# Performance work log

Hardware: AMD Instinct MI355X
Metric: run time of the kernel (lower is better)

Reference implementation:

```python
import jax, jax.numpy as jnp
import numpy as np

N, E = 50000, 800000
MUL, NATTR, NEMB, HID, NPATH = 32, 8, 8, 8, 5
AVG_NEIGH = 16.0
INV3 = 1.0 / np.sqrt(3.0)  # CG norm for 1o x 1o -> 0e (dot)
INV2 = 1.0 / np.sqrt(2.0)  # CG norm for 1o x 1o -> 1o (cross)


def setup_inputs() -> dict:
    key = jax.random.key(0)
    ks = jax.random.split(key, 16)
    f = lambda k, s: jax.random.normal(k, s, jnp.float32)
    return {
        "node_s": f(ks[0], (N, MUL)),
        "node_v": f(ks[1], (N, MUL, 3)),
        "node_attrs": f(ks[2], (N, NATTR)),
        "edge_emb": f(ks[3], (E, NEMB)),
        "edge_sh0": f(ks[4], (E, 1)),
        "edge_sh1": f(ks[5], (E, 3)),
        "W1_s": f(ks[6], (MUL, MUL)),
        "W1_v": f(ks[7], (MUL, MUL)),
        "Wm1": f(ks[8], (NEMB, HID)),
        "Wm2": f(ks[9], (HID, NPATH * MUL)),
        "W2_s": f(ks[10], (2 * MUL, MUL)),
        "W2_v": f(ks[11], (3 * MUL, MUL)),
        "Wsc_s": f(ks[12], (MUL, NATTR, MUL)),
        "Wsc_v": f(ks[13], (MUL, NATTR, MUL)),
        "edge_src": jax.random.randint(ks[14], (E,), 0, N),
        "edge_dst": jax.random.randint(ks[15], (E,), 0, N),
    }


def reference(node_s, node_v, node_attrs, edge_emb, edge_sh0, edge_sh1,
              W1_s, W1_v, Wm1, Wm2, W2_s, W2_v, Wsc_s, Wsc_v,
              edge_src, edge_dst):
    # linear_1: per-l equivariant channel mixing
    x_s = node_s @ W1_s / np.sqrt(MUL)                          # [N, MUL]
    x_v = jnp.einsum('nuc,uv->nvc', node_v, W1_v) / np.sqrt(MUL)  # [N, MUL, 3]
    # gather source node features per edge
    s = x_s[edge_src]   # [E, MUL]
    v = x_v[edge_src]   # [E, MUL, 3]
    # radial MLP on edge embedding -> per-edge UVU tensor-product weights
    h = jax.nn.silu(edge_emb @ Wm1 / np.sqrt(NEMB))
    w = (h @ Wm2 / np.sqrt(HID)).reshape(E, NPATH, MUL)
    w1, w2, w3, w4, w5 = (w[:, i] for i in range(NPATH))
    # UVU Clebsch-Gordan paths (lmax = 1)
    p1 = w1 * s * edge_sh0                                              # 0e x 0e -> 0e
    p2 = w2 * jnp.einsum('euc,ec->eu', v, edge_sh1) * INV3              # 1o x 1o -> 0e
    p3 = w3[:, :, None] * s[:, :, None] * edge_sh1[:, None, :]          # 0e x 1o -> 1o
    p4 = w4[:, :, None] * v * edge_sh0[:, :, None]                      # 1o x 0e -> 1o
    p5 = w5[:, :, None] * jnp.cross(v, edge_sh1[:, None, :]) * INV2     # 1o x 1o -> 1o
    msg_s = jnp.concatenate([p1, p2], axis=1)       # [E, 2*MUL]
    msg_v = jnp.concatenate([p3, p4, p5], axis=1)   # [E, 3*MUL, 3]
    # scatter-add messages to destination nodes
    agg_s = jax.ops.segment_sum(msg_s, edge_dst, num_segments=N)
    agg_v = jax.ops.segment_sum(msg_v, edge_dst, num_segments=N)
    inv = 1.0 / np.sqrt(AVG_NEIGH)
    agg_s = agg_s * inv
    agg_v = agg_v * inv
    # linear_2
    m_s = agg_s @ W2_s / np.sqrt(2 * MUL)
    m_v = jnp.einsum('nuc,uv->nvc', agg_v, W2_v) / np.sqrt(3 * MUL)
    # self connection: fully connected TP with scalar node attrs
    nsc = 1.0 / np.sqrt(MUL * NATTR)
    sc_s = jnp.einsum('nu,na,uav->nv', node_s, node_attrs, Wsc_s) * nsc
    sc_v = jnp.einsum('nuc,na,uav->nvc', node_v, node_attrs, Wsc_v) * nsc
    out_s = m_s + sc_s                  # [N, MUL]
    out_v = m_v + sc_v                  # [N, MUL, 3]
    return jnp.concatenate([out_s, out_v.reshape(N, MUL * 3)], axis=1)  # [N, 128]
```

## Files before the change

### kernel.cpp

```cpp
#include <hip/hip_runtime.h>
#include <math.h>

#define NN 50000
#define NE 800000
#define MUL 32
#define NPB 4
#define SCANB 49

static __device__ __forceinline__ float sigmoidf_(float v) {
    return 1.0f / (1.0f + __expf(-v));
}

#define INV_SQRT_MUL   0.17677669529663687f
#define INV_SQRT_NEMB  0.35355339059327373f
#define INV_SQRT_HID   0.35355339059327373f
#define INV3C          0.5773502691896258f
#define INV2C          0.7071067811865476f
#define INV_NEIGH      0.25f
#define INV_SQRT_2MUL  0.125f
#define INV_SQRT_3MUL  0.10206207261596575f
#define NSC            0.0625f

__global__ __launch_bounds__(256) void k_node(
    const float* __restrict__ node_s, const float* __restrict__ node_v,
    const float* __restrict__ attrs,
    const float* __restrict__ W1_s, const float* __restrict__ W1_v,
    const float* __restrict__ Wsc_s, const float* __restrict__ Wsc_v,
    const int* __restrict__ edge_dst, int* __restrict__ counts,
    float* __restrict__ x, float* __restrict__ out)
{
    __shared__ float nd[NPB][136];
    __shared__ float gs[NPB][1024];
    __shared__ float gv[NPB][1024];
    const int t  = threadIdx.x;
    const int nb = blockIdx.x * NPB;

    {
        int g = blockIdx.x * 256 + t;
        if (g < NE) atomicAdd(&counts[edge_dst[g]], 1);
    }

#pragma unroll
    for (int i = t; i < NPB * 128; i += 256) {
        int nn = i >> 7, j = i & 127;
        nd[nn][j] = (j < 32) ? node_s[(nb + nn) * 32 + j]
                             : node_v[(nb + nn) * 96 + (j - 32)];
    }
    if (t < NPB * 8) nd[t >> 3][128 + (t & 7)] = attrs[(nb + (t >> 3)) * 8 + (t & 7)];
    __syncthreads();

    float at[NPB][8];
#pragma unroll
    for (int nn = 0; nn < NPB; ++nn)
#pragma unroll
        for (int a = 0; a < 8; ++a) at[nn][a] = nd[nn][128 + a];

#pragma unroll
    for (int r = 0; r < 4; ++r) {
        const int idx = t + 256 * r;
        const int u = idx >> 5, vch = idx & 31;
        float as[NPB] = {0.f, 0.f, 0.f, 0.f};
        float av[NPB] = {0.f, 0.f, 0.f, 0.f};
#pragma unroll
        for (int a = 0; a < 8; ++a) {
            const float ws = Wsc_s[(u * 8 + a) * 32 + vch];
            const float wvw = Wsc_v[(u * 8 + a) * 32 + vch];
#pragma unroll
            for (int nn = 0; nn < NPB; ++nn) {
                as[nn] += at[nn][a] * ws;
                av[nn] += at[nn][a] * wvw;
            }
        }
#pragma unroll
        for (int nn = 0; nn < NPB; ++nn) {
            gs[nn][idx] = as[nn];
            gv[nn][idx] = av[nn];
        }
    }
    __syncthreads();

    const int o  = t & 127;
    const int nh = t >> 7;
    if (o < 32) {
        float ax[2] = {0.f, 0.f}, asc[2] = {0.f, 0.f};
#pragma unroll
        for (int uu = 0; uu < 32; ++uu) {
            const float w1 = W1_s[uu * 32 + o];
#pragma unroll
            for (int r2 = 0; r2 < 2; ++r2) {
                const int nn = nh + 2 * r2;
                const float s = nd[nn][uu];
                ax[r2]  += s * w1;
                asc[r2] += s * gs[nn][(uu << 5) + o];
            }
        }
#pragma unroll
        for (int r2 = 0; r2 < 2; ++r2) {
            const int nidx = nb + nh + 2 * r2;
            x[(size_t)nidx * 128 + 4 * o] = ax[r2] * INV_SQRT_MUL;
            out[(size_t)nidx * 128 + o]   = asc[r2] * NSC;
        }
    } else {
        const int q = o - 32;
        const int vch = q / 3, c = q - 3 * vch;
        float ax[2] = {0.f, 0.f}, asc[2] = {0.f, 0.f};
#pragma unroll
        for (int uu = 0; uu < 32; ++uu) {
            const float w1 = W1_v[uu * 32 + vch];
#pragma unroll
            for (int r2 = 0; r2 < 2; ++r2) {
                const int nn = nh + 2 * r2;
                const float vv = nd[nn][32 + 3 * uu + c];
                ax[r2]  += vv * w1;
                asc[r2] += vv * gv[nn][(uu << 5) + vch];
            }
        }
#pragma unroll
        for (int r2 = 0; r2 < 2; ++r2) {
            const int nidx = nb + nh + 2 * r2;
            x[(size_t)nidx * 128 + 4 * vch + 1 + c] = ax[r2] * INV_SQRT_MUL;
            out[(size_t)nidx * 128 + o]             = asc[r2] * NSC;
        }
    }
}

__global__ __launch_bounds__(1024) void k_scan_a(
    const int* __restrict__ counts, int* __restrict__ escan,
    int* __restrict__ bsum)
{
    __shared__ int sh[1024];
    const int t = threadIdx.x;
    const int i = blockIdx.x * 1024 + t;
    int v = (i < NN) ? counts[i] : 0;
    sh[t] = v;
    __syncthreads();
    for (int off = 1; off < 1024; off <<= 1) {
        int u = (t >= off) ? sh[t - off] : 0;
        __syncthreads();
        sh[t] += u;
        __syncthreads();
    }
    if (i < NN) escan[i] = sh[t] - v;
    if (t == 1023) bsum[blockIdx.x] = sh[1023];
}

__global__ __launch_bounds__(1024) void k_scan_c(
    const int* __restrict__ escan, const int* __restrict__ bsum,
    int* __restrict__ offsets, int* __restrict__ cursor)
{
    __shared__ int sbase;
    const int t = threadIdx.x;
    if (t < 64) {
        int v = (t < blockIdx.x) ? bsum[t] : 0;
        for (int off = 32; off > 0; off >>= 1) v += __shfl_xor(v, off, 64);
        if (t == 0) sbase = v;
    }
    __syncthreads();
    const int i = blockIdx.x * 1024 + t;
    if (i == 0) offsets[NN] = NE;
    if (i < NN) {
        int o = sbase + escan[i];
        offsets[i] = o;
        cursor[i] = o;
    }
}

__global__ __launch_bounds__(256) void k_pack(
    const float* __restrict__ edge_emb, const float* __restrict__ edge_sh0,
    const float* __restrict__ edge_sh1,
    const int* __restrict__ edge_src, const int* __restrict__ edge_dst,
    const float* __restrict__ Wm1,
    int* __restrict__ cursor, float* __restrict__ epack)
{
    int e = blockIdx.x * 256 + threadIdx.x;
    if (e >= NE) return;
    const float4* p = (const float4*)(edge_emb + e * 8);
    float4 a = p[0], b = p[1];
    float emb[8] = {a.x, a.y, a.z, a.w, b.x, b.y, b.z, b.w};
    float h[8];
#pragma unroll
    for (int j = 0; j < 8; ++j) {
        float s = 0.f;
#pragma unroll
        for (int k = 0; k < 8; ++k) s += emb[k] * Wm1[k * 8 + j];
        s *= INV_SQRT_NEMB;
        h[j] = s * sigmoidf_(s);
    }
    float sh0 = edge_sh0[e];
    float sx = edge_sh1[3 * e], sy = edge_sh1[3 * e + 1], sz = edge_sh1[3 * e + 2];
    int src = edge_src[e];
    int pos = atomicAdd(&cursor[edge_dst[e]], 1);
    float4* op = (float4*)(epack + (size_t)pos * 16);
    op[0] = make_float4(__int_as_float(src), sh0, sx, sy);
    op[1] = make_float4(sz, h[0], h[1], h[2]);
    op[2] = make_float4(h[3], h[4], h[5], h[6]);
    op[3] = make_float4(h[7], 0.f, 0.f, 0.f);
}

__global__ __launch_bounds__(256) void k_gather(
    const float* __restrict__ x, const float* __restrict__ epack,
    const float* __restrict__ Wm2, const float* __restrict__ W2_s,
    const float* __restrict__ W2_v,
    const int* __restrict__ offsets, float* __restrict__ out)
{
    __shared__ __align__(16) float wsh[2048];
    __shared__ __align__(16) float wvh[3072];
    __shared__ float msg[4][360];

    for (int i = threadIdx.x; i < 512; i += 256)
        ((float4*)wsh)[i] = ((const float4*)W2_s)[i];
    for (int i = threadIdx.x; i < 768; i += 256)
        ((float4*)wvh)[i] = ((const float4*)W2_v)[i];

    const int w    = threadIdx.x >> 6;
    const int L    = threadIdx.x & 63;
    const int u    = L & 31;
    const int half = L >> 5;
    const int n    = blockIdx.x * 4 + w;

    float wc[5][8];
#pragma unroll
    for (int p = 0; p < 5; ++p)
#pragma unroll
        for (int q = 0; q < 8; ++q)
            wc[p][q] = Wm2[q * 160 + p * 32 + u] * INV_SQRT_HID;

    float pa = 0.f, pb = 0.f;
    float p30 = 0.f, p31 = 0.f, p32 = 0.f;
    float p40 = 0.f, p41 = 0.f, p42 = 0.f;
    float p50 = 0.f, p51 = 0.f, p52 = 0.f;

    const int beg = offsets[n];
    const int end = offsets[n + 1];
    const int cnt = end - beg;

#define EDGE_BODY() do { \
        const float sh0 = r0.y, sx = r0.z, sy = r0.w, sz = r1.x; \
        const float w0 = r1.y*wc[0][0] + r1.z*wc[0][1] + r1.w*wc[0][2] + r2.x*wc[0][3] \
                       + r2.y*wc[0][4] + r2.z*wc[0][5] + r2.w*wc[0][6] + h7*wc[0][7]; \
        const float w1 = r1.y*wc[1][0] + r1.z*wc[1][1] + r1.w*wc[1][2] + r2.x*wc[1][3] \
                       + r2.y*wc[1][4] + r2.z*wc[1][5] + r2.w*wc[1][6] + h7*wc[1][7]; \
        const float w2 = r1.y*wc[2][0] + r1.z*wc[2][1] + r1.w*wc[2][2] + r2.x*wc[2][3] \
                       + r2.y*wc[2][4] + r2.z*wc[2][5] + r2.w*wc[2][6] + h7*wc[2][7]; \
        const float w3 = r1.y*wc[3][0] + r1.z*wc[3][1] + r1.w*wc[3][2] + r2.x*wc[3][3] \
                       + r2.y*wc[3][4] + r2.z*wc[3][5] + r2.w*wc[3][6] + h7*wc[3][7]; \
        const float w4 = r1.y*wc[4][0] + r1.z*wc[4][1] + r1.w*wc[4][2] + r2.x*wc[4][3] \
                       + r2.y*wc[4][4] + r2.z*wc[4][5] + r2.w*wc[4][6] + h7*wc[4][7]; \
        const float ls = xv.x, lv0 = xv.y, lv1 = xv.z, lv2 = xv.w; \
        pa += w0 * (ls * sh0); \
        pb += w1 * (lv0 * sx + lv1 * sy + lv2 * sz); \
        const float t2 = w2 * ls; \
        p30 += t2 * sx; p31 += t2 * sy; p32 += t2 * sz; \
        const float t3 = w3 * sh0; \
        p40 += t3 * lv0; p41 += t3 * lv1; p42 += t3 * lv2; \
        p50 += w4 * (lv1 * sz - lv2 * sy); \
        p51 += w4 * (lv2 * sx - lv0 * sz); \
        p52 += w4 * (lv0 * sy - lv1 * sx); \
    } while (0)

    if (cnt > 0) {
        int e = beg + half;
        int le = min(e, end - 1);
        const float4* rp = (const float4*)(epack + (size_t)le * 16);
        float4 r0 = rp[0], r1 = rp[1], r2 = rp[2];
        float  h7 = epack[(size_t)le * 16 + 12];
        float4 xv = *(const float4*)(x + (size_t)__float_as_int(r0.x) * 128 + 4 * u);

        const int np = cnt >> 1;
        for (int it = 0; it < np; ++it) {
            const int pe = min(e + 2, end - 1);
            const float4* qp = (const float4*)(epack + (size_t)pe * 16);
            const float4 q0 = qp[0], q1 = qp[1], q2 = qp[2];
            const float  qh7 = epack[(size_t)pe * 16 + 12];
            const float4 nxv = *(const float4*)(x + (size_t)__float_as_int(q0.x) * 128 + 4 * u);

            EDGE_BODY();

            r0 = q0; r1 = q1; r2 = q2; h7 = qh7; xv = nxv;
            e += 2;
        }
        if (cnt & 1) {
            const float mask = (half == 0) ? 1.f : 0.f;
            r0.y *= mask; r0.z *= mask; r0.w *= mask; r1.x *= mask;
            EDGE_BODY();
        }
    }
#undef EDGE_BODY

    pa  += __shfl_xor(pa, 32);  pb  += __shfl_xor(pb, 32);
    p30 += __shfl_xor(p30, 32); p31 += __shfl_xor(p31, 32); p32 += __shfl_xor(p32, 32);
    p40 += __shfl_xor(p40, 32); p41 += __shfl_xor(p41, 32); p42 += __shfl_xor(p42, 32);
    p50 += __shfl_xor(p50, 32); p51 += __shfl_xor(p51, 32); p52 += __shfl_xor(p52, 32);

    {
        float* mg = msg[w];
        if (half == 0) {
            mg[u]              = pa  * INV_NEIGH;
            mg[32 + u]         = pb  * (INV3C * INV_NEIGH);
            mg[64 + u]         = p30 * INV_NEIGH;
            mg[64 + 96 + u]    = p31 * INV_NEIGH;
            mg[64 + 192 + u]   = p32 * INV_NEIGH;
        } else {
            mg[64 + 32 + u]        = p40 * INV_NEIGH;
            mg[64 + 96 + 32 + u]   = p41 * INV_NEIGH;
            mg[64 + 192 + 32 + u]  = p42 * INV_NEIGH;
            const float f = INV2C * INV_NEIGH;
            mg[64 + 64 + u]        = p50 * f;
            mg[64 + 96 + 64 + u]   = p51 * f;
            mg[64 + 192 + 64 + u]  = p52 * f;
        }
    }
    __syncthreads();

    {
        const int nb = blockIdx.x * 4;
        const int t = threadIdx.x;
        if (t < 128) {
            const int node = t >> 5, o = t & 31;
            float s = 0.f;
#pragma unroll
            for (int uu = 0; uu < 64; ++uu) s += msg[node][uu] * wsh[uu * 32 + o];
            out[(size_t)(nb + node) * 128 + o] += s * INV_SQRT_2MUL;
        } else {
            const int node = (t - 128) >> 5, vch = t & 31;
            float s0 = 0.f, s1 = 0.f, s2 = 0.f;
#pragma unroll
            for (int uu = 0; uu < 96; ++uu) {
                const float wgt = wvh[uu * 32 + vch];
                s0 += msg[node][64 + uu]       * wgt;
                s1 += msg[node][64 + 96 + uu]  * wgt;
                s2 += msg[node][64 + 192 + uu] * wgt;
            }
            float* po = out + (size_t)(nb + node) * 128 + 32 + vch * 3;
            po[0] += s0 * INV_SQRT_3MUL;
            po[1] += s1 * INV_SQRT_3MUL;
            po[2] += s2 * INV_SQRT_3MUL;
        }
    }
}

extern "C" void kernel_launch(void* const* d_in, const int* in_sizes, int n_in,
                              void* d_out, int out_size, void* d_ws, size_t ws_size,
                              hipStream_t stream) {
    const float* node_s   = (const float*)d_in[0];
    const float* node_v   = (const float*)d_in[1];
    const float* attrs    = (const float*)d_in[2];
    const float* edge_emb = (const float*)d_in[3];
    const float* edge_sh0 = (const float*)d_in[4];
    const float* edge_sh1 = (const float*)d_in[5];
    const float* W1_s     = (const float*)d_in[6];
    const float* W1_v     = (const float*)d_in[7];
    const float* Wm1      = (const float*)d_in[8];
    const float* Wm2      = (const float*)d_in[9];
    const float* W2_s     = (const float*)d_in[10];
    const float* W2_v     = (const float*)d_in[11];
    const float* Wsc_s    = (const float*)d_in[12];
    const float* Wsc_v    = (const float*)d_in[13];
    const int*   edge_src = (const int*)d_in[14];
    const int*   edge_dst = (const int*)d_in[15];
    float* out = (float*)d_out;

    float* x     = (float*)d_ws;
    float* epack = x + (size_t)NN * 128;
    int*   counts  = (int*)(epack + (size_t)NE * 16);
    int*   offsets = counts + NN;
    int*   cursor  = offsets + NN + 1;
    int*   escan   = cursor + NN;
    int*   bsum    = escan + NN;

    hipMemsetAsync(counts, 0, NN * sizeof(int), stream);

    k_node<<<NN / NPB, 256, 0, stream>>>(node_s, node_v, attrs,
                                         W1_s, W1_v, Wsc_s, Wsc_v,
                                         edge_dst, counts, x, out);
    k_scan_a<<<SCANB, 1024, 0, stream>>>(counts, escan, bsum);
    k_scan_c<<<SCANB, 1024, 0, stream>>>(escan, bsum, offsets, cursor);
    k_pack<<<(NE + 255) / 256, 256, 0, stream>>>(edge_emb, edge_sh0, edge_sh1,
                                                 edge_src, edge_dst, Wm1,
                                                 cursor, epack);
    k_gather<<<NN / 4, 256, 0, stream>>>(x, epack, Wm2, W2_s, W2_v,
                                         offsets, out);
}
```

Measured before the change: 411.7 us.

## Drop shared W2 staging, deepen edge prefetch, vectorize message layout

Removes the per-block shared-memory copies of W2_s and W2_v and reads them from global/L2 in the final linear, shrinking LDS use and setting launch bounds to 3 blocks per CU. The edge loop now prefetches edge records two iterations ahead, up from one, using pointer arithmetic clamped to the last edge. Vector messages are stored interleaved as float4 so the W2_v contraction does one LDS vector load per uu. This trades a redundant shared-memory fill per block for global weight loads, and raises register pressure from the extra prefetch buffers.

```diff
diff --git a/kernel.cpp b/kernel.cpp
--- a/kernel.cpp
+++ b/kernel.cpp
@@ -197,20 +197,13 @@
     op[3] = make_float4(h[7], 0.f, 0.f, 0.f);
 }
 
-__global__ __launch_bounds__(256) void k_gather(
+__global__ __launch_bounds__(256, 3) void k_gather(
     const float* __restrict__ x, const float* __restrict__ epack,
     const float* __restrict__ Wm2, const float* __restrict__ W2_s,
     const float* __restrict__ W2_v,
     const int* __restrict__ offsets, float* __restrict__ out)
 {
-    __shared__ __align__(16) float wsh[2048];
-    __shared__ __align__(16) float wvh[3072];
-    __shared__ float msg[4][360];
-
-    for (int i = threadIdx.x; i < 512; i += 256)
-        ((float4*)wsh)[i] = ((const float4*)W2_s)[i];
-    for (int i = threadIdx.x; i < 768; i += 256)
-        ((float4*)wvh)[i] = ((const float4*)W2_v)[i];
+    __shared__ __align__(16) float msg[4][452];
 
     const int w    = threadIdx.x >> 6;
     const int L    = threadIdx.x & 63;
@@ -259,25 +252,36 @@
     } while (0)
 
     if (cnt > 0) {
-        int e = beg + half;
-        int le = min(e, end - 1);
-        const float4* rp = (const float4*)(epack + (size_t)le * 16);
-        float4 r0 = rp[0], r1 = rp[1], r2 = rp[2];
-        float  h7 = epack[(size_t)le * 16 + 12];
+        const int np = cnt >> 1;
+        const float* rl = epack + (size_t)(end - 1) * 16;
+        const float* rb = epack + ((size_t)beg + half) * 16;
+        if (rb > rl) rb = rl;
+
+        const float* pB = (rb + 32 <= rl) ? (rb + 32) : rl;
+        float4 r0 = ((const float4*)rb)[0];
+        float4 r1 = ((const float4*)rb)[1];
+        float4 r2 = ((const float4*)rb)[2];
+        float  h7 = rb[12];
+        float4 n0 = ((const float4*)pB)[0];
+        float4 n1 = ((const float4*)pB)[1];
+        float4 n2 = ((const float4*)pB)[2];
+        float  nh7 = pB[12];
         float4 xv = *(const float4*)(x + (size_t)__float_as_int(r0.x) * 128 + 4 * u);
 
-        const int np = cnt >> 1;
         for (int it = 0; it < np; ++it) {
-            const int pe = min(e + 2, end - 1);
-            const float4* qp = (const float4*)(epack + (size_t)pe * 16);
-            const float4 q0 = qp[0], q1 = qp[1], q2 = qp[2];
-            const float  qh7 = epack[(size_t)pe * 16 + 12];
-            const float4 nxv = *(const float4*)(x + (size_t)__float_as_int(q0.x) * 128 + 4 * u);
+            const float* pC = (rb + (size_t)(it + 2) * 32 <= rl)
+                              ? (rb + (size_t)(it + 2) * 32) : rl;
+            const float4 f0 = ((const float4*)pC)[0];
+            const float4 f1 = ((const float4*)pC)[1];
+            const float4 f2 = ((const float4*)pC)[2];
+            const float  fh7 = pC[12];
+            const float4 nxv = *(const float4*)(x + (size_t)__float_as_int(n0.x) * 128 + 4 * u);
 
             EDGE_BODY();
 
-            r0 = q0; r1 = q1; r2 = q2; h7 = qh7; xv = nxv;
-            e += 2;
+            r0 = n0; r1 = n1; r2 = n2; h7 = nh7;
+            n0 = f0; n1 = f1; n2 = f2; nh7 = fh7;
+            xv = nxv;
         }
         if (cnt & 1) {
             const float mask = (half == 0) ? 1.f : 0.f;
@@ -295,19 +299,16 @@
     {
         float* mg = msg[w];
         if (half == 0) {
-            mg[u]              = pa  * INV_NEIGH;
-            mg[32 + u]         = pb  * (INV3C * INV_NEIGH);
-            mg[64 + u]         = p30 * INV_NEIGH;
-            mg[64 + 96 + u]    = p31 * INV_NEIGH;
-            mg[64 + 192 + u]   = p32 * INV_NEIGH;
+            mg[u]      = pa * INV_NEIGH;
+            mg[32 + u] = pb * (INV3C * INV_NEIGH);
+            *(float4*)&mg[64 + 4 * u] =
+                make_float4(p30 * INV_NEIGH, p31 * INV_NEIGH, p32 * INV_NEIGH, 0.f);
         } else {
-            mg[64 + 32 + u]        = p40 * INV_NEIGH;
-            mg[64 + 96 + 32 + u]   = p41 * INV_NEIGH;
-            mg[64 + 192 + 32 + u]  = p42 * INV_NEIGH;
+            *(float4*)&mg[64 + 4 * (32 + u)] =
+                make_float4(p40 * INV_NEIGH, p41 * INV_NEIGH, p42 * INV_NEIGH, 0.f);
             const float f = INV2C * INV_NEIGH;
-            mg[64 + 64 + u]        = p50 * f;
-            mg[64 + 96 + 64 + u]   = p51 * f;
-            mg[64 + 192 + 64 + u]  = p52 * f;
+            *(float4*)&mg[64 + 4 * (64 + u)] =
+                make_float4(p50 * f, p51 * f, p52 * f, 0.f);
         }
     }
     __syncthreads();
@@ -318,18 +319,19 @@
         if (t < 128) {
             const int node = t >> 5, o = t & 31;
             float s = 0.f;
-#pragma unroll
-            for (int uu = 0; uu < 64; ++uu) s += msg[node][uu] * wsh[uu * 32 + o];
+#pragma unroll 16
+            for (int uu = 0; uu < 64; ++uu) s += msg[node][uu] * W2_s[uu * 32 + o];
             out[(size_t)(nb + node) * 128 + o] += s * INV_SQRT_2MUL;
         } else {
             const int node = (t - 128) >> 5, vch = t & 31;
             float s0 = 0.f, s1 = 0.f, s2 = 0.f;
-#pragma unroll
+#pragma unroll 8
             for (int uu = 0; uu < 96; ++uu) {
-                const float wgt = wvh[uu * 32 + vch];
-                s0 += msg[node][64 + uu]       * wgt;
-                s1 += msg[node][64 + 96 + uu]  * wgt;
-                s2 += msg[node][64 + 192 + uu] * wgt;
+                const float wgt = W2_v[uu * 32 + vch];
+                const float4 mv = *(const float4*)&msg[node][64 + 4 * uu];
+                s0 += mv.x * wgt;
+                s1 += mv.y * wgt;
+                s2 += mv.z * wgt;
             }
             float* po = out + (size_t)(nb + node) * 128 + 32 + vch * 3;
             po[0] += s0 * INV_SQRT_3MUL;
```

Result: slower. 447.6 us (+8.7%).
